# Kernel tuning notes

Measured on AMD Instinct MI355X. Metric: run time of the kernel, lower is better.

## Reference

```python
import jax, jax.numpy as jnp
import numpy as np
from jax.scipy.special import logsumexp

G, E, K, D, B, L, M, KN = 32000, 256, 8, 6, 4, 512, 64, 4
STEP, EPS = 0.05, 1.0


def setup_inputs() -> dict:
    key = jax.random.key(0)
    ks = jax.random.split(key, 16)
    s = 0.05  # weight scale for numerical stability
    return {
        'masked': jax.random.randint(ks[0], (B, L), 0, G),
        'unmasked': jax.random.randint(ks[1], (B, L), 0, G),
        'mask': jax.random.randint(ks[2], (B, M), 0, L),
        'summer': jnp.ones((B, M), jnp.float32),
        'embed': jax.random.normal(ks[3], (G, E), jnp.float32) * s,
        'pos': jax.random.normal(ks[4], (L, E), jnp.float32) * s,
        'Wt': jax.random.normal(ks[5], (D, E, E), jnp.float32) * s,
        'Wc': jax.random.normal(ks[6], (D, E, E), jnp.float32) * s,
        'Wq': jax.random.normal(ks[7], (D, K * E, E), jnp.float32) * s,
        'Wd': jax.random.normal(ks[8], (D, K * E, K * E), jnp.float32) * s,
        'Wo': jax.random.normal(ks[9], (D, K * E, E), jnp.float32) * s,
        'Wkc': jax.random.normal(ks[10], (E * KN, E), jnp.float32) * s,
        'bkc': jax.random.normal(ks[11], (E * KN,), jnp.float32) * s,
        'Wem': jax.random.normal(ks[12], (E, E), jnp.float32) * s,
    }


def _norm(x):
    # y / (eps + y.std(-1, unbiased)); torch std is ddof=1
    return x / (EPS + jnp.std(x, axis=-1, ddof=1, keepdims=True))


def reference(masked, unmasked, mask, summer, embed, pos, Wt, Wc, Wq, Wd, Wo, Wkc, bkc, Wem):
    b, l = masked.shape
    # batch init: token + positional embedding, normalized
    xsa = _norm(embed[masked] + pos[None, :l])  # (B,L,E)
    inv_sqrt_e = 1.0 / (E ** 0.5)
    for d in range(D):
        # local transition terms (roll +/- 1 along sequence)
        xsad = jax.nn.relu(jnp.roll(xsa, 1, axis=1) @ Wt[d]) @ Wc[d]
        xsad = xsad + jax.nn.relu(jnp.roll(xsa, -1, axis=1) @ Wc[d].T) @ Wt[d].T
        # QKV_Attention: K query heads against raw xsa keys/values
        q = (xsa @ Wq[d].T).reshape(b, l, K, E)           # (B,L,K,E)
        hijk = jnp.einsum('blke,bme->blkm', q, xsa) * inv_sqrt_e  # (B,L,K,L)
        pijk = jax.nn.softmax(hijk, axis=-1)
        yik = jnp.einsum('blkm,bme->blke', pijk, xsa)      # (B,L,K,E)
        xid = yik.reshape(b, l, K * E)
        # Dense -> ReLU -> Dense (mode 1)
        xidact = jax.nn.relu(xid @ Wd[d].T)                # (B,L,K*E)
        xsad = xsad + xidact @ Wo[d]                       # (B,L,E)
        # gradnorm + residual update + layernorm
        xsad = _norm(xsad)
        xsa = _norm(xsa + STEP * xsad)
    # loss head: gather masked positions
    lptok = jnp.take_along_axis(xsa, mask[:, :, None], axis=1)  # (B,M,E)
    m = mask.shape[1]
    xx = (lptok @ Wkc.T + bkc).reshape(b, m * KN, E)       # kchoice
    xx = jnp.einsum('bne,ble->bnl', xx, xsa)               # (B,M*KN,L)
    xx = jnp.einsum('bnl,ble->bne', xx, xsa)               # (B,M*KN,E)
    logits = (xx @ Wem) @ embed.T                          # (B,M*KN,G)
    k_lp = jax.nn.log_softmax(logits, axis=-1).reshape(b, m, KN, G)
    lp = logsumexp(k_lp, axis=-2) - jnp.float32(np.log(KN))  # (B,M,G)
    tgt = jnp.take_along_axis(unmasked, mask, axis=1)       # (B,M)
    cent = jnp.take_along_axis(lp, tgt[:, :, None], axis=-1)[:, :, 0]
    loss = -(cent * summer).sum(-1) / jnp.clip(summer.sum(-1), 1.0, None)
    return loss
```

## Files before the change

kernel.cpp:

```cpp
#include <hip/hip_runtime.h>
#include <math.h>
#include <stdint.h>

#define G_ 32000
#define E_ 256
#define K_ 8
#define D_ 6
#define B_ 4
#define L_ 512
#define M_ 64
#define KN_ 4
#define STEP_ 0.05f
#define BL_ (B_ * L_)
#define KE_ (K_ * E_)
#define NSPLIT_ 100
#define GCH_ 5

typedef __attribute__((ext_vector_type(8))) short short8;
typedef __attribute__((ext_vector_type(4))) float f32x4;
typedef __attribute__((ext_vector_type(4))) short short4v;

__device__ __forceinline__ short f2bf(float f) {
  unsigned u = __builtin_bit_cast(unsigned, f);
  unsigned r = (u + 0x7fffu + ((u >> 16) & 1u)) >> 16;
  return (short)r;
}
__device__ __forceinline__ float bf2f(short h) {
  return __builtin_bit_cast(float, ((unsigned)(unsigned short)h) << 16);
}

__device__ __forceinline__ void gload16(const void* g, void* l) {
  __builtin_amdgcn_global_load_lds(
      reinterpret_cast<const __attribute__((address_space(1))) void*>(
          reinterpret_cast<uintptr_t>(g)),
      reinterpret_cast<__attribute__((address_space(3))) void*>(
          reinterpret_cast<uintptr_t>(l)),
      16, 0, 0);
}

__device__ __forceinline__ float wsum(float v) {
#pragma unroll
  for (int o = 32; o > 0; o >>= 1) v += __shfl_xor(v, o, 64);
  return v;
}
__device__ __forceinline__ float wmaxr(float v) {
#pragma unroll
  for (int o = 32; o > 0; o >>= 1) v = fmaxf(v, __shfl_xor(v, o, 64));
  return v;
}
__device__ __forceinline__ float block_sum(float v, float* sm) {
  v = wsum(v);
  int wid = threadIdx.x >> 6, lane = threadIdx.x & 63;
  if (lane == 0) sm[wid] = v;
  __syncthreads();
  float r = sm[0] + sm[1] + sm[2] + sm[3];
  __syncthreads();
  return r;
}
__device__ __forceinline__ float block_max(float v, float* sm) {
  v = wmaxr(v);
  int wid = threadIdx.x >> 6, lane = threadIdx.x & 63;
  if (lane == 0) sm[wid] = v;
  __syncthreads();
  float r = fmaxf(fmaxf(sm[0], sm[1]), fmaxf(sm[2], sm[3]));
  __syncthreads();
  return r;
}

template <bool RELU, bool OBF>
__global__ __launch_bounds__(256) void mg128x64_k(
    const short* __restrict__ A, const short* __restrict__ B,
    void* __restrict__ Cg, int Kd, int lda, int ldb, int ldc) {
  __shared__ short As[128 * 64];
  __shared__ short Bs[64 * 64];
  int bid = blockIdx.x;
  int wgid = (bid & 7) * 64 + (bid >> 3);
  int m0 = (wgid & 15) * 128, n0 = (wgid >> 4) * 64;
  int t = threadIdx.x, w = t >> 6, l = t & 63;
  int l16 = l & 15, qd = l >> 4, hi8 = qd * 8;
  int wr_ = w >> 1, wc_ = w & 1;
  int sr = l >> 3;
  int scol = ((l & 7) * 8) ^ (sr << 3);
  f32x4 acc[4][2];
#pragma unroll
  for (int i = 0; i < 4; i++)
#pragma unroll
    for (int j = 0; j < 2; j++) acc[i][j] = {0.f, 0.f, 0.f, 0.f};

  for (int k0 = 0; k0 < Kd; k0 += 64) {
    __syncthreads();
#pragma unroll
    for (int c = 0; c < 4; c++) {
      int sub = w * 4 + c;
      int r = sub * 8 + sr;
      gload16(A + (long)(m0 + r) * lda + k0 + scol, &As[sub * 512]);
    }
#pragma unroll
    for (int c = 0; c < 2; c++) {
      int sub = w * 2 + c;
      int r = sub * 8 + sr;
      gload16(B + (long)(n0 + r) * ldb + k0 + scol, &Bs[sub * 512]);
    }
    __syncthreads();
#pragma unroll
    for (int ks = 0; ks < 2; ks++) {
      short8 af[4], bf[2];
#pragma unroll
      for (int rf = 0; rf < 4; rf++) {
        int row = wr_ * 64 + rf * 16 + l16;
        af[rf] = *(const short8*)&As[(row * 64 + ks * 32 + hi8) ^ ((row & 7) << 3)];
      }
#pragma unroll
      for (int cf = 0; cf < 2; cf++) {
        int row = wc_ * 32 + cf * 16 + l16;
        bf[cf] = *(const short8*)&Bs[(row * 64 + ks * 32 + hi8) ^ ((row & 7) << 3)];
      }
#pragma unroll
      for (int rf = 0; rf < 4; rf++)
#pragma unroll
        for (int cf = 0; cf < 2; cf++)
          acc[rf][cf] = __builtin_amdgcn_mfma_f32_16x16x32_bf16(
              af[rf], bf[cf], acc[rf][cf], 0, 0, 0);
    }
  }
#pragma unroll
  for (int rf = 0; rf < 4; rf++) {
#pragma unroll
    for (int cf = 0; cf < 2; cf++) {
      int col = n0 + wc_ * 32 + cf * 16 + l16;
#pragma unroll
      for (int j = 0; j < 4; j++) {
        int row = m0 + wr_ * 64 + rf * 16 + qd * 4 + j;
        float v = acc[rf][cf][j];
        if (RELU) v = fmaxf(v, 0.f);
        long idx = (long)row * ldc + col;
        if (OBF) ((short*)Cg)[idx] = f2bf(v);
        else ((float*)Cg)[idx] = v;
      }
    }
  }
}

__global__ __launch_bounds__(256) void mg64sk_k(
    const short* __restrict__ A, const short* __restrict__ B,
    float* __restrict__ P, int Klen, int lda, int ldb, int ldc, long pstride) {
  __shared__ short As[64 * 64];
  __shared__ short Bs[64 * 64];
  int z = blockIdx.z;
  int kbase = z * Klen;
  int m0 = blockIdx.y * 64, n0 = blockIdx.x * 64;
  int t = threadIdx.x, w = t >> 6, l = t & 63;
  int l16 = l & 15, qd = l >> 4, hi8 = qd * 8;
  int wr_ = w >> 1, wc_ = w & 1;
  int sr = l >> 3;
  int scol = ((l & 7) * 8) ^ (sr << 3);
  f32x4 acc[2][2];
#pragma unroll
  for (int i = 0; i < 2; i++)
#pragma unroll
    for (int j = 0; j < 2; j++) acc[i][j] = {0.f, 0.f, 0.f, 0.f};

  for (int k0 = 0; k0 < Klen; k0 += 64) {
    __syncthreads();
#pragma unroll
    for (int c = 0; c < 2; c++) {
      int sub = w * 2 + c;
      int r = sub * 8 + sr;
      gload16(A + (long)(m0 + r) * lda + kbase + k0 + scol, &As[sub * 512]);
      gload16(B + (long)(n0 + r) * ldb + kbase + k0 + scol, &Bs[sub * 512]);
    }
    __syncthreads();
#pragma unroll
    for (int ks = 0; ks < 2; ks++) {
      short8 af[2], bf[2];
#pragma unroll
      for (int rf = 0; rf < 2; rf++) {
        int row = wr_ * 32 + rf * 16 + l16;
        af[rf] = *(const short8*)&As[(row * 64 + ks * 32 + hi8) ^ ((row & 7) << 3)];
      }
#pragma unroll
      for (int cf = 0; cf < 2; cf++) {
        int row = wc_ * 32 + cf * 16 + l16;
        bf[cf] = *(const short8*)&Bs[(row * 64 + ks * 32 + hi8) ^ ((row & 7) << 3)];
      }
#pragma unroll
      for (int rf = 0; rf < 2; rf++)
#pragma unroll
        for (int cf = 0; cf < 2; cf++)
          acc[rf][cf] = __builtin_amdgcn_mfma_f32_16x16x32_bf16(
              af[rf], bf[cf], acc[rf][cf], 0, 0, 0);
    }
  }
  float* Pz = P + z * pstride;
#pragma unroll
  for (int rf = 0; rf < 2; rf++) {
#pragma unroll
    for (int cf = 0; cf < 2; cf++) {
      int col = n0 + wc_ * 32 + cf * 16 + l16;
#pragma unroll
      for (int j = 0; j < 4; j++) {
        int row = m0 + wr_ * 32 + rf * 16 + qd * 4 + j;
        Pz[(long)row * ldc + col] = acc[rf][cf][j];
      }
    }
  }
}

template <bool BIAS>
__global__ __launch_bounds__(256) void mgh_k(
    const short* __restrict__ Ag, const short* __restrict__ Bg,
    short* __restrict__ Cg, const float* __restrict__ bias, int Kd, int lda,
    int ldb, int ldc, long sA, long sB, long sC) {
  __shared__ short As[64 * 64];
  __shared__ short Bs[64 * 64];
  int z = blockIdx.z;
  const short* A = Ag + z * sA;
  const short* B = Bg + z * sB;
  short* C = Cg + z * sC;
  int m0 = blockIdx.y * 64, n0 = blockIdx.x * 64;
  int t = threadIdx.x, w = t >> 6, l = t & 63;
  int l16 = l & 15, qd = l >> 4, hi8 = qd * 8;
  int wr_ = w >> 1, wc_ = w & 1;
  int sr = l >> 3;
  int scol = ((l & 7) * 8) ^ (sr << 3);
  f32x4 acc[2][2];
#pragma unroll
  for (int i = 0; i < 2; i++)
#pragma unroll
    for (int j = 0; j < 2; j++) acc[i][j] = {0.f, 0.f, 0.f, 0.f};

  for (int k0 = 0; k0 < Kd; k0 += 64) {
    __syncthreads();
#pragma unroll
    for (int c = 0; c < 2; c++) {
      int sub = w * 2 + c;
      int r = sub * 8 + sr;
      gload16(A + (long)(m0 + r) * lda + k0 + scol, &As[sub * 512]);
      gload16(B + (long)(n0 + r) * ldb + k0 + scol, &Bs[sub * 512]);
    }
    __syncthreads();
#pragma unroll
    for (int ks = 0; ks < 2; ks++) {
      short8 af[2], bf[2];
#pragma unroll
      for (int rf = 0; rf < 2; rf++) {
        int row = wr_ * 32 + rf * 16 + l16;
        af[rf] = *(const short8*)&As[(row * 64 + ks * 32 + hi8) ^ ((row & 7) << 3)];
      }
#pragma unroll
      for (int cf = 0; cf < 2; cf++) {
        int row = wc_ * 32 + cf * 16 + l16;
        bf[cf] = *(const short8*)&Bs[(row * 64 + ks * 32 + hi8) ^ ((row & 7) << 3)];
      }
#pragma unroll
      for (int rf = 0; rf < 2; rf++)
#pragma unroll
        for (int cf = 0; cf < 2; cf++)
          acc[rf][cf] = __builtin_amdgcn_mfma_f32_16x16x32_bf16(
              af[rf], bf[cf], acc[rf][cf], 0, 0, 0);
    }
  }
#pragma unroll
  for (int rf = 0; rf < 2; rf++) {
#pragma unroll
    for (int cf = 0; cf < 2; cf++) {
      int col = n0 + wc_ * 32 + cf * 16 + l16;
      float bv = BIAS ? bias[col] : 0.f;
#pragma unroll
      for (int j = 0; j < 4; j++) {
        int row = m0 + wr_ * 32 + rf * 16 + qd * 4 + j;
        C[(long)row * ldc + col] = f2bf(acc[rf][cf][j] + bv);
      }
    }
  }
}

__global__ __launch_bounds__(256) void tpair_k(
    const short* __restrict__ xsa_bf, const short* __restrict__ wtT,
    const short* __restrict__ wcb, short* __restrict__ T) {
  __shared__ short As[64 * 64];
  __shared__ short Bs[64 * 64];
  int z = blockIdx.z;
  const short* Bb = z ? wcb : wtT;
  int rollv = z ? -1 : 1;
  int m0 = blockIdx.y * 64, n0 = blockIdx.x * 64;
  int t = threadIdx.x, w = t >> 6, l = t & 63;
  int l16 = l & 15, qd = l >> 4, hi8 = qd * 8;
  int wr_ = w >> 1, wc_ = w & 1;
  int sr = l >> 3;
  int scol = ((l & 7) * 8) ^ (sr << 3);
  f32x4 acc[2][2];
#pragma unroll
  for (int i = 0; i < 2; i++)
#pragma unroll
    for (int j = 0; j < 2; j++) acc[i][j] = {0.f, 0.f, 0.f, 0.f};
  for (int k0 = 0; k0 < E_; k0 += 64) {
    __syncthreads();
#pragma unroll
    for (int c = 0; c < 2; c++) {
      int sub = w * 2 + c;
      int r = sub * 8 + sr;
      int gr = m0 + r;
      int bb = gr >> 9, pp = gr & (L_ - 1);
      gr = (bb << 9) | ((pp - rollv + L_) & (L_ - 1));
      gload16(xsa_bf + (long)gr * E_ + k0 + scol, &As[sub * 512]);
      gload16(Bb + (long)(n0 + r) * E_ + k0 + scol, &Bs[sub * 512]);
    }
    __syncthreads();
#pragma unroll
    for (int ks = 0; ks < 2; ks++) {
      short8 af[2], bf[2];
#pragma unroll
      for (int rf = 0; rf < 2; rf++) {
        int row = wr_ * 32 + rf * 16 + l16;
        af[rf] = *(const short8*)&As[(row * 64 + ks * 32 + hi8) ^ ((row & 7) << 3)];
      }
#pragma unroll
      for (int cf = 0; cf < 2; cf++) {
        int row = wc_ * 32 + cf * 16 + l16;
        bf[cf] = *(const short8*)&Bs[(row * 64 + ks * 32 + hi8) ^ ((row & 7) << 3)];
      }
#pragma unroll
      for (int rf = 0; rf < 2; rf++)
#pragma unroll
        for (int cf = 0; cf < 2; cf++)
          acc[rf][cf] = __builtin_amdgcn_mfma_f32_16x16x32_bf16(
              af[rf], bf[cf], acc[rf][cf], 0, 0, 0);
    }
  }
#pragma unroll
  for (int rf = 0; rf < 2; rf++) {
#pragma unroll
    for (int cf = 0; cf < 2; cf++) {
      int col = n0 + wc_ * 32 + cf * 16 + l16;
#pragma unroll
      for (int j = 0; j < 4; j++) {
        int row = m0 + wr_ * 32 + rf * 16 + qd * 4 + j;
        T[(long)row * 512 + z * 256 + col] = f2bf(fmaxf(acc[rf][cf][j], 0.f));
      }
    }
  }
}

__global__ __launch_bounds__(512, 2) void flash3_k(
    const short* __restrict__ q_bf, const short* __restrict__ xsa_bf,
    const short* __restrict__ xsaT_bf, short* __restrict__ y_bf) {
  __shared__ short smem[69888];
  float* Obuf = (float*)smem;
  float* mst = (float*)&smem[69632];
  float* lst = mst + 64;
  int q0 = blockIdx.x * 64, hk = blockIdx.y, b = blockIdx.z;
  int t = threadIdx.x, w = t >> 6, l = t & 63;
  int l16 = l & 15, qd = l >> 4, hi8 = qd * 8;
  int qb = w & 3, half = w >> 2;
  const float scale = 0.0625f;

  short8 qf[8];
  {
    const short* qrow =
        q_bf + (long)(b * L_ + q0 + qb * 16 + l16) * KE_ + hk * 256;
#pragma unroll
    for (int ks = 0; ks < 8; ks++)
      qf[ks] = *(const short8*)(qrow + ks * 32 + hi8);
  }
  f32x4 acc_o[16];
#pragma unroll
  for (int i = 0; i < 16; i++) acc_o[i] = {0.f, 0.f, 0.f, 0.f};
  float mreg[4], lreg[4];
#pragma unroll
  for (int j = 0; j < 4; j++) { mreg[j] = -1e30f; lreg[j] = 0.f; }

  auto STAGE = [&](int nbuf, int it) {
#pragma unroll
    for (int c = 0; c < 4; c++) {
      int ch = w * 4 + c, hh = ch >> 4, rp = ch & 15;
      int row = rp * 2 + (l >> 5);
      int colsw = ((l & 31) * 8) ^ ((row & 7) << 3);
      gload16(xsa_bf + (long)(b * L_ + hh * 256 + it * 32 + row) * E_ + colsw,
              &smem[(nbuf * 2 + hh) * 8192 + rp * 512]);
    }
#pragma unroll
    for (int c = 0; c < 4; c++) {
      int ch = w * 4 + c, hh = ch >> 4, rg = ch & 15;
      int er = rg * 16 + (l >> 2);
      int col = (l & 3) * 8;
      gload16(xsaT_bf + (long)(b * E_ + er) * L_ + hh * 256 + it * 32 + col,
              &smem[32768 + (nbuf * 2 + hh) * 8192 + rg * 512]);
    }
  };

  STAGE(0, 0);
  __syncthreads();
  int cur = 0;
  for (int it = 0; it < 8; it++) {
    if (it < 7) STAGE(cur ^ 1, it + 1);
    const short* Kb = &smem[(cur * 2 + half) * 8192];
    const short* Vb = &smem[32768 + (cur * 2 + half) * 8192];
    short* Pw = &smem[65536 + w * 512];
    f32x4 s4[2];
    s4[0] = {0.f, 0.f, 0.f, 0.f};
    s4[1] = {0.f, 0.f, 0.f, 0.f};
    __builtin_amdgcn_s_setprio(1);
#pragma unroll
    for (int ks = 0; ks < 8; ks++) {
#pragma unroll
      for (int cf = 0; cf < 2; cf++) {
        int row = cf * 16 + l16;
        short8 kb = *(const short8*)&Kb[row * 256 +
                                        ((ks * 32 + hi8) ^ ((row & 7) << 3))];
        s4[cf] = __builtin_amdgcn_mfma_f32_16x16x32_bf16(qf[ks], kb, s4[cf], 0, 0, 0);
      }
    }
    __builtin_amdgcn_s_setprio(0);
    float alpha[4];
#pragma unroll
    for (int j = 0; j < 4; j++) {
      float v0 = s4[0][j] * scale, v1 = s4[1][j] * scale;
      float rmax = fmaxf(v0, v1);
#pragma unroll
      for (int mk = 1; mk <= 8; mk <<= 1) rmax = fmaxf(rmax, __shfl_xor(rmax, mk, 64));
      float mn = fmaxf(mreg[j], rmax);
      float p0 = __expf(v0 - mn), p1 = __expf(v1 - mn);
      float ps = p0 + p1;
#pragma unroll
      for (int mk = 1; mk <= 8; mk <<= 1) ps += __shfl_xor(ps, mk, 64);
      alpha[j] = __expf(mreg[j] - mn);
      lreg[j] = lreg[j] * alpha[j] + ps;
      mreg[j] = mn;
      int r = qd * 4 + j;
      Pw[r * 32 + l16] = f2bf(p0);
      Pw[r * 32 + 16 + l16] = f2bf(p1);
    }
#pragma unroll
    for (int cfo = 0; cfo < 16; cfo++)
#pragma unroll
      for (int j = 0; j < 4; j++) acc_o[cfo][j] *= alpha[j];
    short8 pa = *(const short8*)&Pw[l16 * 32 + hi8];
    __builtin_amdgcn_s_setprio(1);
#pragma unroll
    for (int cfo = 0; cfo < 16; cfo++) {
      int er = cfo * 16 + l16;
      short8 vb = *(const short8*)&Vb[er * 32 + hi8];
      acc_o[cfo] = __builtin_amdgcn_mfma_f32_16x16x32_bf16(pa, vb, acc_o[cfo], 0, 0, 0);
    }
    __builtin_amdgcn_s_setprio(0);
    __syncthreads();
    cur ^= 1;
  }
  if (half == 1) {
#pragma unroll
    for (int cfo = 0; cfo < 16; cfo++)
#pragma unroll
      for (int j = 0; j < 4; j++)
        Obuf[qb * 4096 + (qd * 4 + j) * 256 + cfo * 16 + l16] = acc_o[cfo][j];
    if (l16 == 0) {
#pragma unroll
      for (int j = 0; j < 4; j++) {
        mst[qb * 16 + qd * 4 + j] = mreg[j];
        lst[qb * 16 + qd * 4 + j] = lreg[j];
      }
    }
  }
  __syncthreads();
  if (half == 0) {
#pragma unroll
    for (int j = 0; j < 4; j++) {
      int r = qd * 4 + j;
      float m1 = mst[qb * 16 + r], l1 = lst[qb * 16 + r];
      float mn = fmaxf(mreg[j], m1);
      float a0 = __expf(mreg[j] - mn), a1 = __expf(m1 - mn);
      float linv = 1.0f / (lreg[j] * a0 + l1 * a1);
      short* yrow = y_bf + (long)(b * L_ + q0 + qb * 16 + r) * KE_ + hk * 256;
#pragma unroll
      for (int cfo = 0; cfo < 16; cfo++) {
        float o1 = Obuf[qb * 4096 + r * 256 + cfo * 16 + l16];
        yrow[cfo * 16 + l16] = f2bf((acc_o[cfo][j] * a0 + o1 * a1) * linv);
      }
    }
  }
}

__global__ __launch_bounds__(256) void finish_k(
    const float* __restrict__ Ptr, const float* __restrict__ Pwo,
    float* __restrict__ xsa, short* __restrict__ xsa_bf,
    short* __restrict__ xsaT_bf) {
  long r = blockIdx.x;
  int b = (int)(r / L_), ll = (int)(r % L_);
  int t = threadIdx.x;
  __shared__ float sm[4];
  long off = r * E_ + t;
  const long ps = (long)BL_ * E_;
  float vd = Ptr[off] + Ptr[ps + off] + Pwo[off] + Pwo[ps + off] +
             Pwo[2 * ps + off] + Pwo[3 * ps + off];
  float s1 = block_sum(vd, sm);
  float s2 = block_sum(vd * vd, sm);
  float mean = s1 * (1.0f / E_);
  float var = (s2 - s1 * mean) * (1.0f / (E_ - 1));
  float vdn = vd / (1.0f + sqrtf(fmaxf(var, 0.f)));
  float u = xsa[off] + STEP_ * vdn;
  s1 = block_sum(u, sm);
  s2 = block_sum(u * u, sm);
  mean = s1 * (1.0f / E_);
  var = (s2 - s1 * mean) * (1.0f / (E_ - 1));
  float xn = u / (1.0f + sqrtf(fmaxf(var, 0.f)));
  xsa[off] = xn;
  short h = f2bf(xn);
  xsa_bf[off] = h;
  xsaT_bf[((long)b * E_ + t) * L_ + ll] = h;
}

__global__ __launch_bounds__(256) void lse2_k(
    const short* __restrict__ tmat_bf, const short* __restrict__ embed_bf,
    float* __restrict__ mpart, float* __restrict__ spart) {
  __shared__ short Bs[64 * 256];
  int split = blockIdx.x, rb = blockIdx.y;
  int t = threadIdx.x, w = t >> 6, l = t & 63;
  int l16 = l & 15, qd = l >> 4, hi8 = qd * 8;
  short8 areg[8];
  {
    const short* ar = tmat_bf + (long)(rb * 64 + w * 16 + l16) * E_;
#pragma unroll
    for (int ks = 0; ks < 8; ks++) areg[ks] = *(const short8*)(ar + ks * 32 + hi8);
  }
  float m[4], s[4];
#pragma unroll
  for (int j = 0; j < 4; j++) { m[j] = -1e30f; s[j] = 0.f; }
  long gbase = (long)split * (GCH_ * 64);
  for (int ch = 0; ch < GCH_; ch++) {
    long g0 = gbase + ch * 64;
    __syncthreads();
#pragma unroll
    for (int j = 0; j < 8; j++) {
      int sub = w * 8 + j;
      int r = sub * 2 + (l >> 5);
      int col = ((l & 31) * 8) ^ ((r & 7) << 3);
      gload16(embed_bf + (g0 + r) * E_ + col, &Bs[sub * 512]);
    }
    __syncthreads();
    f32x4 acc[4];
#pragma unroll
    for (int cf = 0; cf < 4; cf++) acc[cf] = {0.f, 0.f, 0.f, 0.f};
    __builtin_amdgcn_s_setprio(1);
#pragma unroll
    for (int ks = 0; ks < 8; ks++) {
#pragma unroll
      for (int cf = 0; cf < 4; cf++) {
        int row = cf * 16 + l16;
        short8 b = *(const short8*)&Bs[(row * 256 + ks * 32 + hi8) ^ ((row & 7) << 3)];
        acc[cf] = __builtin_amdgcn_mfma_f32_16x16x32_bf16(areg[ks], b, acc[cf], 0, 0, 0);
      }
    }
    __builtin_amdgcn_s_setprio(0);
#pragma unroll
    for (int j = 0; j < 4; j++) {
      float vm = fmaxf(fmaxf(acc[0][j], acc[1][j]), fmaxf(acc[2][j], acc[3][j]));
      float mn = fmaxf(m[j], vm);
      s[j] = s[j] * __expf(m[j] - mn) + __expf(acc[0][j] - mn) +
             __expf(acc[1][j] - mn) + __expf(acc[2][j] - mn) +
             __expf(acc[3][j] - mn);
      m[j] = mn;
    }
  }
#pragma unroll
  for (int j = 0; j < 4; j++) {
#pragma unroll
    for (int mask = 1; mask <= 8; mask <<= 1) {
      float mo = __shfl_xor(m[j], mask, 64);
      float so = __shfl_xor(s[j], mask, 64);
      float mn = fmaxf(m[j], mo);
      s[j] = s[j] * __expf(m[j] - mn) + so * __expf(mo - mn);
      m[j] = mn;
    }
    if (l16 == 0) {
      int row = rb * 64 + w * 16 + qd * 4 + j;
      mpart[(long)row * NSPLIT_ + split] = m[j];
      spart[(long)row * NSPLIT_ + split] = s[j];
    }
  }
}

__device__ __forceinline__ void cvt8n_blk(const float* __restrict__ src,
                                          short* __restrict__ dst, int blk,
                                          int nblk, int t) {
#pragma unroll
  for (int r = 0; r < 4; r++) {
    long i = (long)(blk + r * nblk) * 256 + t;
    const float4* s4 = (const float4*)src;
    float4 a = s4[2 * i], b = s4[2 * i + 1];
    short8 o = {f2bf(a.x), f2bf(a.y), f2bf(a.z), f2bf(a.w),
                f2bf(b.x), f2bf(b.y), f2bf(b.z), f2bf(b.w)};
    ((short8*)dst)[i] = o;
  }
}
__device__ __forceinline__ void trans64_blk(const float* __restrict__ src,
                                            short* __restrict__ dst, int bx,
                                            int by, int C, int ldd,
                                            short (*tile)[68], int t) {
  int c0 = bx * 64, r0 = by * 64;
  int tr = t >> 4;
  int tc = (t & 15) * 4;
#pragma unroll
  for (int k = 0; k < 4; k++) {
    int r = tr + k * 16;
    float4 v = *(const float4*)(src + (long)(r0 + r) * C + c0 + tc);
    tile[r][tc + 0] = f2bf(v.x);
    tile[r][tc + 1] = f2bf(v.y);
    tile[r][tc + 2] = f2bf(v.z);
    tile[r][tc + 3] = f2bf(v.w);
  }
  __syncthreads();
#pragma unroll
  for (int j = 0; j < 2; j++) {
    int ch = t + j * 256;
    int rd = ch >> 3;
    int cd = (ch & 7) * 8;
    short8 o;
#pragma unroll
    for (int e = 0; e < 8; e++) o[e] = tile[cd + e][rd];
    *(short8*)(dst + (long)(c0 + rd) * ldd + r0 + cd) = o;
  }
}
#define WCVT_BLKS (1000 + 32 + 6 * 592 + 16 + 6 * 160)
__global__ __launch_bounds__(256) void wcvt_all_k(
    const float* __restrict__ embed, const float* __restrict__ Wt,
    const float* __restrict__ Wc, const float* __restrict__ Wq,
    const float* __restrict__ Wd, const float* __restrict__ Wo,
    const float* __restrict__ Wkc, const float* __restrict__ Wem,
    short* embed_bf, short* wcb, short* wq, short* wd, short* wtT, short* woT,
    short* wcat, short* wkc_bf, short* wemT) {
  __shared__ short tile[64][68];
  int blk = blockIdx.x, t = threadIdx.x;
  if (blk < 1000) { cvt8n_blk(embed, embed_bf, blk, 1000, t); return; }
  blk -= 1000;
  if (blk < 32) { cvt8n_blk(Wkc, wkc_bf, blk, 32, t); return; }
  blk -= 32;
  if (blk < 6 * 592) {
    int d = blk / 592;
    int r = blk - d * 592;
    if (r < 512) { cvt8n_blk(Wd + (long)d * KE_ * KE_, wd + (long)d * KE_ * KE_, r, 512, t); return; }
    r -= 512;
    if (r < 64) { cvt8n_blk(Wq + (long)d * KE_ * E_, wq + (long)d * KE_ * E_, r, 64, t); return; }
    r -= 64;
    if (r < 8) { cvt8n_blk(Wc + (long)d * E_ * E_, wcb + (long)d * E_ * E_, r, 8, t); return; }
    r -= 8;
    {
      const float* Wt_d = Wt + (long)d * E_ * E_;
      short* wcat_d = wcat + (long)d * E_ * 512;
#pragma unroll
      for (int it = 0; it < 4; it++) {
        long i = (long)(r + it * 8) * 256 + t;
        int n = (int)(i >> 5);
        int kc = (int)(i & 31) * 8;
        float4 a = *(const float4*)(Wt_d + (long)n * E_ + kc);
        float4 b = *(const float4*)(Wt_d + (long)n * E_ + kc + 4);
        short8 o = {f2bf(a.x), f2bf(a.y), f2bf(a.z), f2bf(a.w),
                    f2bf(b.x), f2bf(b.y), f2bf(b.z), f2bf(b.w)};
        *(short8*)(wcat_d + (long)n * 512 + 256 + kc) = o;
      }
      return;
    }
  }
  blk -= 6 * 592;
  if (blk < 16) { trans64_blk(Wem, wemT, blk & 3, blk >> 2, E_, E_, tile, t); return; }
  blk -= 16;
  {
    int d = blk / 160;
    int r = blk - d * 160;
    if (r < 16) {
      trans64_blk(Wt + (long)d * E_ * E_, wtT + (long)d * E_ * E_, r & 3,
                  r >> 2, E_, E_, tile, t);
      return;
    }
    r -= 16;
    if (r < 128) {
      trans64_blk(Wo + (long)d * KE_ * E_, woT + (long)d * E_ * KE_, r & 3,
                  r >> 2, E_, KE_, tile, t);
      return;
    }
    r -= 128;
    trans64_blk(Wc + (long)d * E_ * E_, wcat + (long)d * E_ * 512, r & 3,
                r >> 2, E_, 512, tile, t);
  }
}

__global__ __launch_bounds__(256) void embed_init_k(
    const int* __restrict__ masked, const float* __restrict__ embed,
    const float* __restrict__ pos, float* __restrict__ xsa,
    short* __restrict__ xsa_bf, short* __restrict__ xsaT_bf) {
  int bl = blockIdx.x;
  int b = bl / L_, ll = bl % L_;
  int t = threadIdx.x;
  __shared__ float sm[4];
  int tok = masked[bl];
  float v = embed[(long)tok * E_ + t] + pos[(long)ll * E_ + t];
  float s1 = block_sum(v, sm);
  float s2 = block_sum(v * v, sm);
  float mean = s1 * (1.0f / E_);
  float var = (s2 - s1 * mean) * (1.0f / (E_ - 1));
  float xn = v / (1.0f + sqrtf(fmaxf(var, 0.f)));
  xsa[(long)bl * E_ + t] = xn;
  short h = f2bf(xn);
  xsa_bf[(long)bl * E_ + t] = h;
  xsaT_bf[((long)b * E_ + t) * L_ + ll] = h;
}

__global__ __launch_bounds__(256) void gatherbf_k(const short* __restrict__ xsa_bf,
                                                  const int* __restrict__ mask,
                                                  short* __restrict__ lptok_bf) {
  int bm = blockIdx.x;
  int b = bm >> 6;
  int t = threadIdx.x;
  int p = mask[bm];
  lptok_bf[(long)bm * E_ + t] = xsa_bf[((long)b * L_ + p) * E_ + t];
}

__global__ __launch_bounds__(256) void cent_k(
    const short* __restrict__ tmat_bf, const float* __restrict__ embed,
    const int* __restrict__ mask, const int* __restrict__ unmasked,
    const float* __restrict__ mpart, const float* __restrict__ spart,
    float* __restrict__ cent) {
  int bm = blockIdx.x;
  int b = bm >> 6, m = bm & 63;
  int t = threadIdx.x;
  __shared__ float sm[4];
  __shared__ float tlv[KN_];
  int pos = mask[bm];
  int tgt = unmasked[b * L_ + pos];
  float ev = embed[(long)tgt * E_ + t];
  for (int kn = 0; kn < KN_; kn++) {
    long grow = (long)b * (M_ * KN_) + m * KN_ + kn;
    float tv = bf2f(tmat_bf[grow * E_ + t]);
    float dot = block_sum(tv * ev, sm);
    float m2 = (t < NSPLIT_) ? mpart[grow * NSPLIT_ + t] : -1e30f;
    float s2 = (t < NSPLIT_) ? spart[grow * NSPLIT_ + t] : 0.f;
    float Mx = block_max(m2, sm);
    float S = block_sum(s2 * __expf(m2 - Mx), sm);
    if (t == 0) tlv[kn] = dot - (Mx + __logf(S));
  }
  __syncthreads();
  if (t == 0) {
    float mx = fmaxf(fmaxf(tlv[0], tlv[1]), fmaxf(tlv[2], tlv[3]));
    float s = __expf(tlv[0] - mx) + __expf(tlv[1] - mx) + __expf(tlv[2] - mx) +
              __expf(tlv[3] - mx);
    cent[bm] = __logf(s) + mx - 1.3862943611198906f;
  }
}

__global__ __launch_bounds__(256) void loss_k(const float* __restrict__ cent,
                                              const float* __restrict__ summer,
                                              float* __restrict__ out) {
  int t = threadIdx.x;
  int b = t >> 6, m = t & 63;
  float c = cent[b * 64 + m], su = summer[b * 64 + m];
  float num = wsum(c * su);
  float den = wsum(su);
  if (m == 0) out[b] = -num / fmaxf(den, 1.0f);
}

extern "C" void kernel_launch(void* const* d_in, const int* in_sizes, int n_in,
                              void* d_out, int out_size, void* d_ws,
                              size_t ws_size, hipStream_t stream) {
  (void)in_sizes; (void)n_in; (void)out_size; (void)ws_size;
  const int* masked = (const int*)d_in[0];
  const int* unmasked = (const int*)d_in[1];
  const int* mask = (const int*)d_in[2];
  const float* summer = (const float*)d_in[3];
  const float* embed = (const float*)d_in[4];
  const float* pos = (const float*)d_in[5];
  const float* Wt = (const float*)d_in[6];
  const float* Wc = (const float*)d_in[7];
  const float* Wq = (const float*)d_in[8];
  const float* Wd = (const float*)d_in[9];
  const float* Wo = (const float*)d_in[10];
  const float* Wkc = (const float*)d_in[11];
  const float* bkc = (const float*)d_in[12];
  const float* Wem = (const float*)d_in[13];
  float* out = (float*)d_out;

  char* p = (char*)d_ws;
  auto take = [&](size_t bytes) {
    char* r = p;
    p += (bytes + 255) & ~(size_t)255;
    return r;
  };
  float* xsa = (float*)take((size_t)BL_ * E_ * 4);
  short* xsa_bf = (short*)take((size_t)BL_ * E_ * 2);
  short* xsaT_bf = (short*)take((size_t)BL_ * E_ * 2);
  short* t_buf = (short*)take((size_t)BL_ * 512 * 2);
  short* q_bf = (short*)take((size_t)BL_ * KE_ * 2);
  short* y_bf = (short*)take((size_t)BL_ * KE_ * 2);
  float* P_tr = (float*)take((size_t)2 * BL_ * E_ * 4);
  float* P_wo = (float*)take((size_t)4 * BL_ * E_ * 4);
  short* wcb = (short*)take((size_t)D_ * E_ * E_ * 2);
  short* wtT = (short*)take((size_t)D_ * E_ * E_ * 2);
  short* wq = (short*)take((size_t)D_ * KE_ * E_ * 2);
  short* wd = (short*)take((size_t)D_ * KE_ * KE_ * 2);
  short* woT = (short*)take((size_t)D_ * E_ * KE_ * 2);
  short* wcat = (short*)take((size_t)D_ * E_ * 512 * 2);
  short* wkc_bf = (short*)take((size_t)KN_ * E_ * E_ * 2);
  short* wemT = (short*)take((size_t)E_ * E_ * 2);
  short* embed_bf = (short*)take((size_t)G_ * E_ * 2);
  short* lptok_bf = (short*)take((size_t)B_ * M_ * E_ * 2);
  short* xx1_bf = (short*)take((size_t)B_ * M_ * KN_ * E_ * 2);
  short* xx2_bf = (short*)take((size_t)B_ * M_ * KN_ * L_ * 2);
  short* xx3_bf = (short*)take((size_t)B_ * M_ * KN_ * E_ * 2);
  short* tmat_bf = (short*)take((size_t)B_ * M_ * KN_ * E_ * 2);
  float* mpart = (float*)take((size_t)1024 * NSPLIT_ * 4);
  float* spart = (float*)take((size_t)1024 * NSPLIT_ * 4);
  float* cent = (float*)take((size_t)B_ * M_ * 4);

  dim3 blk(256);
  wcvt_all_k<<<WCVT_BLKS, blk, 0, stream>>>(embed, Wt, Wc, Wq, Wd, Wo, Wkc, Wem,
                                            embed_bf, wcb, wq, wd, wtT, woT,
                                            wcat, wkc_bf, wemT);
  embed_init_k<<<BL_, blk, 0, stream>>>(masked, embed, pos, xsa, xsa_bf, xsaT_bf);

  for (int d = 0; d < D_; d++) {
    short* wcb_d = wcb + (long)d * E_ * E_;
    short* wtT_d = wtT + (long)d * E_ * E_;
    short* wq_d = wq + (long)d * KE_ * E_;
    short* wd_d = wd + (long)d * KE_ * KE_;
    short* woT_d = woT + (long)d * E_ * KE_;
    short* wcat_d = wcat + (long)d * E_ * 512;

    tpair_k<<<dim3(4, 32, 2), blk, 0, stream>>>(xsa_bf, wtT_d, wcb_d, t_buf);
    mg64sk_k<<<dim3(4, 32, 2), blk, 0, stream>>>(t_buf, wcat_d, P_tr, 256, 512,
                                                 512, E_, (long)BL_ * E_);
    mg128x64_k<false, true><<<512, blk, 0, stream>>>(xsa_bf, wq_d, q_bf, E_, E_,
                                                     E_, KE_);
    flash3_k<<<dim3(L_ / 64, K_, B_), dim3(512), 0, stream>>>(q_bf, xsa_bf,
                                                              xsaT_bf, y_bf);
    mg128x64_k<true, true><<<512, blk, 0, stream>>>(y_bf, wd_d, q_bf, KE_, KE_,
                                                    KE_, KE_);
    mg64sk_k<<<dim3(4, 32, 4), blk, 0, stream>>>(q_bf, woT_d, P_wo, 512, KE_,
                                                 KE_, E_, (long)BL_ * E_);
    finish_k<<<BL_, blk, 0, stream>>>(P_tr, P_wo, xsa, xsa_bf, xsaT_bf);
  }

  gatherbf_k<<<B_ * M_, blk, 0, stream>>>(xsa_bf, mask, lptok_bf);
  mgh_k<true><<<dim3(16, 4, 1), blk, 0, stream>>>(
      lptok_bf, wkc_bf, xx1_bf, bkc, E_, E_, E_, KN_ * E_, 0, 0, 0);
  mgh_k<false><<<dim3(8, 4, B_), blk, 0, stream>>>(
      xx1_bf, xsa_bf, xx2_bf, nullptr, E_, E_, E_, L_,
      (long)M_ * KN_ * E_, (long)L_ * E_, (long)M_ * KN_ * L_);
  mgh_k<false><<<dim3(4, 4, B_), blk, 0, stream>>>(
      xx2_bf, xsaT_bf, xx3_bf, nullptr, L_, L_, L_, E_,
      (long)M_ * KN_ * L_, (long)E_ * L_, (long)M_ * KN_ * E_);
  mgh_k<false><<<dim3(4, 16, 1), blk, 0, stream>>>(
      xx3_bf, wemT, tmat_bf, nullptr, E_, E_, E_, E_, 0, 0, 0);
  lse2_k<<<dim3(NSPLIT_, 16), blk, 0, stream>>>(tmat_bf, embed_bf, mpart, spart);
  cent_k<<<B_ * M_, blk, 0, stream>>>(tmat_bf, embed, mask, unmasked, mpart,
                                      spart, cent);
  loss_k<<<1, blk, 0, stream>>>(cent, summer, out);
}
```

Measured before the change: 681.5 us.

## Fuse Q projection into flash attention kernel and simplify GEMM block mapping

```diff
diff --git a/kernel.cpp b/kernel.cpp
--- a/kernel.cpp
+++ b/kernel.cpp
@@ -73,9 +73,7 @@
     void* __restrict__ Cg, int Kd, int lda, int ldb, int ldc) {
   __shared__ short As[128 * 64];
   __shared__ short Bs[64 * 64];
-  int bid = blockIdx.x;
-  int wgid = (bid & 7) * 64 + (bid >> 3);
-  int m0 = (wgid & 15) * 128, n0 = (wgid >> 4) * 64;
+  int m0 = blockIdx.y * 128, n0 = blockIdx.x * 64;
   int t = threadIdx.x, w = t >> 6, l = t & 63;
   int l16 = l & 15, qd = l >> 4, hi8 = qd * 8;
   int wr_ = w >> 1, wc_ = w & 1;
@@ -342,8 +340,8 @@
   }
 }
 
-__global__ __launch_bounds__(512, 2) void flash3_k(
-    const short* __restrict__ q_bf, const short* __restrict__ xsa_bf,
+__global__ __launch_bounds__(512, 2) void flash4_k(
+    const short* __restrict__ xsa_bf, const short* __restrict__ wq,
     const short* __restrict__ xsaT_bf, short* __restrict__ y_bf) {
   __shared__ short smem[69888];
   float* Obuf = (float*)smem;
@@ -355,14 +353,62 @@
   int qb = w & 3, half = w >> 2;
   const float scale = 0.0625f;
 
+  short* Albuf = smem;
+  short* Bqbuf = smem + 16384;
+  short* Qbuf = smem + 32768;
+  {
+    const short* asrc = xsa_bf + (long)(b * L_ + q0) * E_;
+#pragma unroll
+    for (int rep = 0; rep < 4; rep++) {
+      int idx = rep * 512 + t;
+      int row = idx >> 5;
+      int cs = (idx & 31) * 8;
+      gload16(asrc + (long)row * E_ + (cs ^ ((row & 7) << 3)), Albuf + (size_t)idx * 8);
+    }
+  }
+  for (int c = 0; c < 4; c++) {
+    const short* bsrc = wq + (long)(hk * 256 + c * 64) * E_;
+#pragma unroll
+    for (int rep = 0; rep < 4; rep++) {
+      int idx = rep * 512 + t;
+      int row = idx >> 5;
+      int cs = (idx & 31) * 8;
+      gload16(bsrc + (long)row * E_ + (cs ^ ((row & 7) << 3)), Bqbuf + (size_t)idx * 8);
+    }
+    __syncthreads();
+    f32x4 fq[2];
+    fq[0] = {0.f, 0.f, 0.f, 0.f};
+    fq[1] = {0.f, 0.f, 0.f, 0.f};
+#pragma unroll
+    for (int ks = 0; ks < 8; ks++) {
+      int ar = qb * 16 + l16;
+      short8 a = *(const short8*)&Albuf[(ar * 256 + ks * 32 + hi8) ^ ((ar & 7) << 3)];
+#pragma unroll
+      for (int cf = 0; cf < 2; cf++) {
+        int br = half * 32 + cf * 16 + l16;
+        short8 bq = *(const short8*)&Bqbuf[(br * 256 + ks * 32 + hi8) ^ ((br & 7) << 3)];
+        fq[cf] = __builtin_amdgcn_mfma_f32_16x16x32_bf16(a, bq, fq[cf], 0, 0, 0);
+      }
+    }
+#pragma unroll
+    for (int cf = 0; cf < 2; cf++)
+#pragma unroll
+      for (int j = 0; j < 4; j++) {
+        int qr = qb * 16 + qd * 4 + j;
+        int qc = c * 64 + half * 32 + cf * 16 + l16;
+        Qbuf[(qr * 256 + qc) ^ ((qr & 7) << 3)] = f2bf(fq[cf][j]);
+      }
+    __syncthreads();
+  }
   short8 qf[8];
   {
-    const short* qrow =
-        q_bf + (long)(b * L_ + q0 + qb * 16 + l16) * KE_ + hk * 256;
+    int qr = qb * 16 + l16;
 #pragma unroll
     for (int ks = 0; ks < 8; ks++)
-      qf[ks] = *(const short8*)(qrow + ks * 32 + hi8);
-  }
+      qf[ks] = *(const short8*)&Qbuf[(qr * 256 + ks * 32 + hi8) ^ ((qr & 7) << 3)];
+  }
+  __syncthreads();
+
   f32x4 acc_o[16];
 #pragma unroll
   for (int i = 0; i < 16; i++) acc_o[i] = {0.f, 0.f, 0.f, 0.f};
@@ -787,7 +833,7 @@
   short* xsa_bf = (short*)take((size_t)BL_ * E_ * 2);
   short* xsaT_bf = (short*)take((size_t)BL_ * E_ * 2);
   short* t_buf = (short*)take((size_t)BL_ * 512 * 2);
-  short* q_bf = (short*)take((size_t)BL_ * KE_ * 2);
+  short* xid_bf = (short*)take((size_t)BL_ * KE_ * 2);
   short* y_bf = (short*)take((size_t)BL_ * KE_ * 2);
   float* P_tr = (float*)take((size_t)2 * BL_ * E_ * 4);
   float* P_wo = (float*)take((size_t)4 * BL_ * E_ * 4);
@@ -826,13 +872,11 @@
     tpair_k<<<dim3(4, 32, 2), blk, 0, stream>>>(xsa_bf, wtT_d, wcb_d, t_buf);
     mg64sk_k<<<dim3(4, 32, 2), blk, 0, stream>>>(t_buf, wcat_d, P_tr, 256, 512,
                                                  512, E_, (long)BL_ * E_);
-    mg128x64_k<false, true><<<512, blk, 0, stream>>>(xsa_bf, wq_d, q_bf, E_, E_,
-                                                     E_, KE_);
-    flash3_k<<<dim3(L_ / 64, K_, B_), dim3(512), 0, stream>>>(q_bf, xsa_bf,
+    flash4_k<<<dim3(L_ / 64, K_, B_), dim3(512), 0, stream>>>(xsa_bf, wq_d,
                                                               xsaT_bf, y_bf);
-    mg128x64_k<true, true><<<512, blk, 0, stream>>>(y_bf, wd_d, q_bf, KE_, KE_,
-                                                    KE_, KE_);
-    mg64sk_k<<<dim3(4, 32, 4), blk, 0, stream>>>(q_bf, woT_d, P_wo, 512, KE_,
+    mg128x64_k<true, true><<<dim3(32, 16), blk, 0, stream>>>(
+        y_bf, wd_d, xid_bf, KE_, KE_, KE_, KE_);
+    mg64sk_k<<<dim3(4, 32, 4), blk, 0, stream>>>(xid_bf, woT_d, P_wo, 512, KE_,
                                                  KE_, E_, (long)BL_ * E_);
     finish_k<<<BL_, blk, 0, stream>>>(P_tr, P_wo, xsa, xsa_bf, xsaT_bf);
   }
```

Result: faster. 663.9 us, median of 2 (-2.6%).
